# Performance work log

Hardware: AMD Instinct MI355X
Metric: run time of the kernel (lower is better)

The kernel has to match this reference:

```python
import jax, jax.numpy as jnp
import numpy as np

B, S, D = 2, 2048, 1024
H = 16
DH = D // H


def _layernorm(x, g, b, eps=1e-5):
    mu = jnp.mean(x, axis=-1, keepdims=True)
    var = jnp.var(x, axis=-1, keepdims=True)
    return (x - mu) * jax.lax.rsqrt(var + eps) * g + b


def setup_inputs() -> dict:
    key = jax.random.key(0)
    ks = jax.random.split(key, 8)
    s = lambda fan_in: 1.0 / np.sqrt(fan_in)
    return {
        "x": jax.random.normal(ks[0], (B, S, D), dtype=jnp.float32),
        "ln1_g": jnp.ones((D,), jnp.float32),
        "ln1_b": jnp.zeros((D,), jnp.float32),
        "w_qkv": jax.random.uniform(ks[1], (D, 3 * D), jnp.float32, -s(D), s(D)),
        "b_qkv": jnp.zeros((3 * D,), jnp.float32),
        "w_out": jax.random.uniform(ks[2], (D, D), jnp.float32, -s(D), s(D)),
        "b_out": jnp.zeros((D,), jnp.float32),
        "ln2_g": jnp.ones((D,), jnp.float32),
        "ln2_b": jnp.zeros((D,), jnp.float32),
        "w1": jax.random.uniform(ks[3], (D, 4 * D), jnp.float32, -s(D), s(D)),
        "b1": jnp.zeros((4 * D,), jnp.float32),
        "w2": jax.random.uniform(ks[4], (4 * D, D), jnp.float32, -s(4 * D), s(4 * D)),
        "b2": jnp.zeros((D,), jnp.float32),
    }


def reference(x, ln1_g, ln1_b, w_qkv, b_qkv, w_out, b_out,
              ln2_g, ln2_b, w1, b1, w2, b2):
    scale = DH ** -0.5
    residual = x
    h = _layernorm(x, ln1_g, ln1_b)
    qkv = h @ w_qkv + b_qkv                      # [B,S,3D]
    q, k, v = jnp.split(qkv, 3, axis=-1)
    # [B,S,D] -> [B,H,S,DH]
    split_heads = lambda t: t.reshape(B, S, H, DH).transpose(0, 2, 1, 3)
    q, k, v = map(split_heads, (q, k, v))
    scores = jnp.einsum("bhsd,bhtd->bhst", q, k) * scale  # full O(S^2) matrix
    attn = jax.nn.softmax(scores, axis=-1)
    out = jnp.einsum("bhst,bhtd->bhsd", attn, v)
    out = out.transpose(0, 2, 1, 3).reshape(B, S, D)
    out = out @ w_out + b_out                    # dropout is identity at eval
    x = residual + out
    residual = x
    h = _layernorm(x, ln2_g, ln2_b)
    h = jax.nn.gelu(h @ w1 + b1, approximate=False)
    h = h @ w2 + b2
    return residual + h
```

## Files before the change

kernel.cpp:

```cpp
#include <hip/hip_runtime.h>
#include <hip/hip_bf16.h>
#include <math.h>

#define Bc 2
#define Sc 2048
#define Dc 1024
#define Hc 16
#define DHc 64
#define Mc (Bc*Sc)

typedef __attribute__((ext_vector_type(8))) short bf16x8;
typedef __attribute__((ext_vector_type(4))) float f32x4;

#define QSCALE 0.18033688f

__device__ __forceinline__ ushort f2bf(float f){
  union { float f; uint32_t u; } c; c.f = f;
  uint32_t u = c.u;
  return (ushort)((u + 0x7fffu + ((u >> 16) & 1u)) >> 16);
}
__device__ __forceinline__ float fast_exp2(float x){
#if __has_builtin(__builtin_amdgcn_exp2f)
  return __builtin_amdgcn_exp2f(x);
#else
  return exp2f(x);
#endif
}
__device__ __forceinline__ float fast_rcp(float x){
#if __has_builtin(__builtin_amdgcn_rcpf)
  return __builtin_amdgcn_rcpf(x);
#else
  return 1.0f / x;
#endif
}
__device__ __forceinline__ float fast_gelu(float x){
  float x2 = x * x;
  float y  = x * (2.30220826f + 0.10294442f * x2);
  float t  = fast_exp2(fminf(y, 80.f));
  return x * t * fast_rcp(t + 1.0f);
}
__device__ __forceinline__ uint32_t cvt_pk_bf16(float a, float b){
  uint32_t r;
  asm("v_cvt_pk_bf16_f32 %0, %1, %2" : "=v"(r) : "v"(a), "v"(b));
  return r;
}

__device__ __forceinline__ void stage16(const void* g, void* lbase, int lane){
#if __has_builtin(__builtin_amdgcn_global_load_lds)
  __builtin_amdgcn_global_load_lds(
      (const __attribute__((address_space(1))) void*)g,
      (__attribute__((address_space(3))) void*)lbase, 16, 0, 0);
#else
  *(int4*)((char*)lbase + lane*16) = *(const int4*)g;
#endif
}

__global__ __launch_bounds__(256) void tcast(const float* __restrict__ w,
                                             ushort* __restrict__ wt,
                                             int K, int N){
  __shared__ float t[32][33];
  int kb = blockIdx.y * 32, nb = blockIdx.x * 32;
  int tx = threadIdx.x & 31, ty = threadIdx.x >> 5;
  #pragma unroll
  for (int i = 0; i < 4; i++)
    t[ty + 8*i][tx] = w[(size_t)(kb + ty + 8*i) * N + nb + tx];
  __syncthreads();
  #pragma unroll
  for (int i = 0; i < 4; i++)
    wt[(size_t)(nb + ty + 8*i) * K + kb + tx] = f2bf(t[tx][ty + 8*i]);
}

__global__ __launch_bounds__(256) void ln_bf16(const float* __restrict__ x,
                                               const float* __restrict__ g,
                                               const float* __restrict__ b,
                                               ushort* __restrict__ out){
  int row = blockIdx.x;
  const float4 xv = reinterpret_cast<const float4*>(x + (size_t)row * Dc)[threadIdx.x];
  float s  = xv.x + xv.y + xv.z + xv.w;
  float sq = xv.x*xv.x + xv.y*xv.y + xv.z*xv.z + xv.w*xv.w;
  #pragma unroll
  for (int m = 1; m < 64; m <<= 1){ s += __shfl_xor(s, m); sq += __shfl_xor(sq, m); }
  __shared__ float ss[4], ssq[4];
  int wv = threadIdx.x >> 6;
  if ((threadIdx.x & 63) == 0){ ss[wv] = s; ssq[wv] = sq; }
  __syncthreads();
  s  = ss[0] + ss[1] + ss[2] + ss[3];
  sq = ssq[0] + ssq[1] + ssq[2] + ssq[3];
  float mu  = s * (1.0f / Dc);
  float var = sq * (1.0f / Dc) - mu * mu;
  float rstd = rsqrtf(var + 1e-5f);
  float4 gv = reinterpret_cast<const float4*>(g)[threadIdx.x];
  float4 bv = reinterpret_cast<const float4*>(b)[threadIdx.x];
  ushort o[4];
  o[0] = f2bf((xv.x - mu) * rstd * gv.x + bv.x);
  o[1] = f2bf((xv.y - mu) * rstd * gv.y + bv.y);
  o[2] = f2bf((xv.z - mu) * rstd * gv.z + bv.z);
  o[3] = f2bf((xv.w - mu) * rstd * gv.w + bv.w);
  *reinterpret_cast<uint2*>(out + (size_t)row * Dc + threadIdx.x * 4) =
      *reinterpret_cast<uint2*>(o);
}

template<int EPI>
__global__ __launch_bounds__(256) void gemm128(
    const ushort* __restrict__ A, const ushort* __restrict__ BT,
    const float* __restrict__ bias,
    ushort* __restrict__ outb,
    ushort* __restrict__ oq, ushort* __restrict__ ok, ushort* __restrict__ ov,
    int N, int K){
  __shared__ short As[2][128*64];
  __shared__ short Bs[2][128*64];

  const int fid = blockIdx.x;
  const int q8 = gridDim.x >> 3;
  const int id2 = (fid & 7) * q8 + (fid >> 3);
  const int nbx = N / 128;
  const int nb = id2 % nbx, mb = id2 / nbx;

  const int tid = threadIdx.x;
  const int wave = tid >> 6, lane = tid & 63;
  const int wm = wave >> 1, wn = wave & 1;
  const int lr = lane & 15, lg = lane >> 4;

  f32x4 acc[4][4] = {};

  const int srow = wave * 8 + (lane >> 3);
  const int sgc  = ((lane & 7) ^ (lane >> 3)) * 8;
  const ushort* Ag = A  + (size_t)(mb * 128 + srow) * K + sgc;
  const ushort* Bg = BT + (size_t)(nb * 128 + srow) * K + sgc;
  const int nK = K >> 6;

  {
    char* Ab = (char*)&As[0][0] + wave * 1024;
    char* Bb = (char*)&Bs[0][0] + wave * 1024;
    #pragma unroll
    for (int c = 0; c < 4; c++){
      stage16(Ag + (size_t)c * 32 * K, Ab + c * 4096, lane);
      stage16(Bg + (size_t)c * 32 * K, Bb + c * 4096, lane);
    }
  }
  __syncthreads();

  const int swzr = (lr & 7) * 8;

  for (int kt = 0; kt < nK; ++kt){
    const int cur = kt & 1;
    if (kt + 1 < nK){
      const int ko = (kt + 1) * 64;
      char* Ab = (char*)&As[cur ^ 1][0] + wave * 1024;
      char* Bb = (char*)&Bs[cur ^ 1][0] + wave * 1024;
      #pragma unroll
      for (int c = 0; c < 4; c++){
        stage16(Ag + (size_t)c * 32 * K + ko, Ab + c * 4096, lane);
        stage16(Bg + (size_t)c * 32 * K + ko, Bb + c * 4096, lane);
      }
    }
    #pragma unroll
    for (int ks = 0; ks < 2; ks++){
      const int col = (ks * 32 + lg * 8) ^ swzr;
      bf16x8 af[4], bfr[4];
      #pragma unroll
      for (int mt = 0; mt < 4; mt++)
        af[mt] = *reinterpret_cast<const bf16x8*>(&As[cur][(wm*64 + mt*16 + lr)*64 + col]);
      #pragma unroll
      for (int nt = 0; nt < 4; nt++)
        bfr[nt] = *reinterpret_cast<const bf16x8*>(&Bs[cur][(wn*64 + nt*16 + lr)*64 + col]);
      #pragma unroll
      for (int mt = 0; mt < 4; mt++)
        #pragma unroll
        for (int nt = 0; nt < 4; nt++)
          acc[mt][nt] = __builtin_amdgcn_mfma_f32_16x16x32_bf16(af[mt], bfr[nt], acc[mt][nt], 0, 0, 0);
    }
    __syncthreads();
  }

  if (EPI == 0){
    #pragma unroll
    for (int mt = 0; mt < 4; mt++){
      const int gm0 = mb * 128 + wm * 64 + mt * 16 + lg * 4;
      const int bb = gm0 >> 11, s0 = gm0 & 2047;
      #pragma unroll
      for (int nt = 0; nt < 4; nt++){
        const int gn = nb * 128 + wn * 64 + nt * 16 + lr;
        const float bv = bias[gn];
        const int p = gn >> 10, d = gn & 1023;
        const int hh = d >> 6, dh = d & 63;
        const int bh = bb * Hc + hh;
        if (p == 2){
          ushort pk[4];
          #pragma unroll
          for (int r = 0; r < 4; r++) pk[r] = f2bf(acc[mt][nt][r] + bv);
          *reinterpret_cast<uint2*>(ov + ((size_t)bh * DHc + dh) * Sc + s0) =
              *reinterpret_cast<uint2*>(pk);
        } else if (p == 0){
          #pragma unroll
          for (int r = 0; r < 4; r++)
            oq[((size_t)bh * Sc + s0 + r) * DHc + dh] = f2bf((acc[mt][nt][r] + bv) * QSCALE);
        } else {
          #pragma unroll
          for (int r = 0; r < 4; r++)
            ok[((size_t)bh * Sc + s0 + r) * DHc + dh] = f2bf(acc[mt][nt][r] + bv);
        }
      }
    }
  } else {
    #pragma unroll
    for (int mt = 0; mt < 4; mt++){
      #pragma unroll
      for (int nt = 0; nt < 4; nt++){
        #pragma unroll
        for (int r = 0; r < 4; r++){
          const int gm = mb * 128 + wm * 64 + mt * 16 + lg * 4 + r;
          const int gn = nb * 128 + wn * 64 + nt * 16 + lr;
          outb[(size_t)gm * N + gn] = f2bf(fast_gelu(acc[mt][nt][r] + bias[gn]));
        }
      }
    }
  }
}

__global__ __launch_bounds__(256) void gemm_res64(
    const ushort* __restrict__ A, const ushort* __restrict__ BT,
    const float* __restrict__ bias, const float* __restrict__ res,
    float* __restrict__ outf, int N, int K){
  __shared__ short As[2][128*64];
  __shared__ short Bs[2][64*64];

  const int fid = blockIdx.x;
  const int q8 = gridDim.x >> 3;
  const int id2 = (fid & 7) * q8 + (fid >> 3);
  const int nbx = N / 64;
  const int nb = id2 % nbx, mb = id2 / nbx;

  const int tid = threadIdx.x;
  const int wave = tid >> 6, lane = tid & 63;
  const int wm = wave >> 1, wn = wave & 1;
  const int lr = lane & 15, lg = lane >> 4;

  f32x4 acc[4][2] = {};

  const int srow = wave * 8 + (lane >> 3);
  const int sgc  = ((lane & 7) ^ (lane >> 3)) * 8;
  const ushort* Ag = A  + (size_t)(mb * 128 + srow) * K + sgc;
  const ushort* Bg = BT + (size_t)(nb * 64  + srow) * K + sgc;
  const int nK = K >> 6;

  {
    char* Ab = (char*)&As[0][0] + wave * 1024;
    char* Bb = (char*)&Bs[0][0] + wave * 1024;
    #pragma unroll
    for (int c = 0; c < 4; c++)
      stage16(Ag + (size_t)c * 32 * K, Ab + c * 4096, lane);
    #pragma unroll
    for (int c = 0; c < 2; c++)
      stage16(Bg + (size_t)c * 32 * K, Bb + c * 4096, lane);
  }
  __syncthreads();

  const int swzr = (lr & 7) * 8;

  for (int kt = 0; kt < nK; ++kt){
    const int cur = kt & 1;
    if (kt + 1 < nK){
      const int ko = (kt + 1) * 64;
      char* Ab = (char*)&As[cur ^ 1][0] + wave * 1024;
      char* Bb = (char*)&Bs[cur ^ 1][0] + wave * 1024;
      #pragma unroll
      for (int c = 0; c < 4; c++)
        stage16(Ag + (size_t)c * 32 * K + ko, Ab + c * 4096, lane);
      #pragma unroll
      for (int c = 0; c < 2; c++)
        stage16(Bg + (size_t)c * 32 * K + ko, Bb + c * 4096, lane);
    }
    #pragma unroll
    for (int ks = 0; ks < 2; ks++){
      const int col = (ks * 32 + lg * 8) ^ swzr;
      bf16x8 af[4], bfr[2];
      #pragma unroll
      for (int mt = 0; mt < 4; mt++)
        af[mt] = *reinterpret_cast<const bf16x8*>(&As[cur][(wm*64 + mt*16 + lr)*64 + col]);
      #pragma unroll
      for (int nt = 0; nt < 2; nt++)
        bfr[nt] = *reinterpret_cast<const bf16x8*>(&Bs[cur][(wn*32 + nt*16 + lr)*64 + col]);
      #pragma unroll
      for (int mt = 0; mt < 4; mt++)
        #pragma unroll
        for (int nt = 0; nt < 2; nt++)
          acc[mt][nt] = __builtin_amdgcn_mfma_f32_16x16x32_bf16(af[mt], bfr[nt], acc[mt][nt], 0, 0, 0);
    }
    __syncthreads();
  }

  #pragma unroll
  for (int mt = 0; mt < 4; mt++){
    #pragma unroll
    for (int nt = 0; nt < 2; nt++){
      #pragma unroll
      for (int r = 0; r < 4; r++){
        const int gm = mb * 128 + wm * 64 + mt * 16 + lg * 4 + r;
        const int gn = nb * 64 + wn * 32 + nt * 16 + lr;
        const size_t i = (size_t)gm * N + gn;
        outf[i] = acc[mt][nt][r] + bias[gn] + res[i];
      }
    }
  }
}

__global__ __launch_bounds__(256) void flash_attn(const ushort* __restrict__ q,
                                                  const ushort* __restrict__ k,
                                                  const ushort* __restrict__ vt,
                                                  ushort* __restrict__ ctx){
  const int bh = blockIdx.y;
  const int q0 = blockIdx.x * 64;
  const int b  = bh >> 4, h = bh & 15;
  const int tid = threadIdx.x, wave = tid >> 6, lane = tid & 63;
  const int lr = lane & 15, lg = lane >> 4;

  __shared__ short Kt[2][64*64];
  __shared__ short Vt[64*64];
  __shared__ short Ps[4][16][68];

  const int g8  = lane & 7;
  const int kr0 = wave * 8 + (lane >> 3);
  const int kcol = (g8 ^ (kr0 & 7)) * 8;
  const ushort* kg0 = k + (size_t)bh * Sc * DHc + (size_t)kr0 * DHc + kcol;
  const ushort* kg1 = kg0 + 32 * DHc;
  char* Kl = (char*)&Kt[0][0] + wave * 1024;
  const int KBUFB = 64 * 64 * 2;

  const int vrow = tid >> 3, vg8 = tid & 7;
  const int vcol = (vg8 ^ (vrow & 7)) * 8;
  const ushort* vg0 = vt + (size_t)bh * DHc * Sc + (size_t)vrow * Sc + vcol;
  const ushort* vg1 = vg0 + (size_t)32 * Sc;

  bf16x8 qf0, qf1;
  {
    const ushort* qp = q + (size_t)bh * Sc * DHc + (size_t)(q0 + wave * 16 + lr) * DHc + lg * 8;
    qf0 = *reinterpret_cast<const bf16x8*>(qp);
    qf1 = *reinterpret_cast<const bf16x8*>(qp + 32);
  }

  f32x4 o[4] = {};
  float lps = 0.f;
  constexpr int NTILES = Sc / 64;

  stage16(kg0, Kl,        lane);
  stage16(kg1, Kl + 4096, lane);
  {
    int4 w0 = *reinterpret_cast<const int4*>(vg0);
    int4 w1 = *reinterpret_cast<const int4*>(vg1);
    *reinterpret_cast<int4*>((char*)&Vt[0] + tid * 16)        = w0;
    *reinterpret_cast<int4*>((char*)&Vt[0] + 4096 + tid * 16) = w1;
  }
  __syncthreads();

  const int swz = (lr & 7) * 8;

  for (int kt = 0; kt < NTILES; ++kt){
    const int cur = kt & 1;
    int4 vr0, vr1;
    if (kt + 1 < NTILES){
      const int nx = (cur ^ 1) * KBUFB;
      stage16(kg0 + (size_t)(kt + 1) * 64 * DHc, Kl + nx,        lane);
      stage16(kg1 + (size_t)(kt + 1) * 64 * DHc, Kl + nx + 4096, lane);
      vr0 = *reinterpret_cast<const int4*>(vg0 + (kt + 1) * 64);
      vr1 = *reinterpret_cast<const int4*>(vg1 + (kt + 1) * 64);
    }

    f32x4 sacc[4];
    __builtin_amdgcn_s_setprio(1);
    #pragma unroll
    for (int nt = 0; nt < 4; nt++){
      const int rb = (nt * 16 + lr) * 64;
      bf16x8 b0 = *reinterpret_cast<const bf16x8*>(&Kt[cur][rb + ((lg * 8) ^ swz)]);
      bf16x8 b1 = *reinterpret_cast<const bf16x8*>(&Kt[cur][rb + ((32 + lg * 8) ^ swz)]);
      f32x4 z = {0.f, 0.f, 0.f, 0.f};
      z = __builtin_amdgcn_mfma_f32_16x16x32_bf16(b0, qf0, z, 0, 0, 0);
      z = __builtin_amdgcn_mfma_f32_16x16x32_bf16(b1, qf1, z, 0, 0, 0);
      sacc[nt] = z;
    }
    __builtin_amdgcn_s_setprio(0);

    #pragma unroll
    for (int nt = 0; nt < 4; nt++){
      float p0 = fast_exp2(sacc[nt][0]);
      float p1 = fast_exp2(sacc[nt][1]);
      float p2 = fast_exp2(sacc[nt][2]);
      float p3 = fast_exp2(sacc[nt][3]);
      lps += (p0 + p1) + (p2 + p3);
      uint2 wd;
      wd.x = cvt_pk_bf16(p0, p1);
      wd.y = cvt_pk_bf16(p2, p3);
      *reinterpret_cast<uint2*>(&Ps[wave][lr][nt * 16 + lg * 4]) = wd;
    }

    bf16x8 pf0 = *reinterpret_cast<const bf16x8*>(&Ps[wave][lr][lg * 8]);
    bf16x8 pf1 = *reinterpret_cast<const bf16x8*>(&Ps[wave][lr][32 + lg * 8]);
    __builtin_amdgcn_s_setprio(1);
    #pragma unroll
    for (int nt = 0; nt < 4; nt++){
      const int rb = (nt * 16 + lr) * 64;
      bf16x8 v0 = *reinterpret_cast<const bf16x8*>(&Vt[rb + ((lg * 8) ^ swz)]);
      bf16x8 v1 = *reinterpret_cast<const bf16x8*>(&Vt[rb + ((32 + lg * 8) ^ swz)]);
      o[nt] = __builtin_amdgcn_mfma_f32_16x16x32_bf16(pf0, v0, o[nt], 0, 0, 0);
      o[nt] = __builtin_amdgcn_mfma_f32_16x16x32_bf16(pf1, v1, o[nt], 0, 0, 0);
    }
    __builtin_amdgcn_s_setprio(0);

    __syncthreads();
    if (kt + 1 < NTILES){
      *reinterpret_cast<int4*>((char*)&Vt[0] + tid * 16)        = vr0;
      *reinterpret_cast<int4*>((char*)&Vt[0] + 4096 + tid * 16) = vr1;
      __syncthreads();
    }
  }

  lps += __shfl_xor(lps, 16);
  lps += __shfl_xor(lps, 32);

  #pragma unroll
  for (int j = 0; j < 4; j++){
    float inv = 1.0f / __shfl(lps, lg * 4 + j);
    int s = q0 + wave * 16 + lg * 4 + j;
    ushort* op = ctx + ((size_t)b * Sc + s) * Dc + h * DHc;
    #pragma unroll
    for (int nt = 0; nt < 4; nt++)
      op[nt * 16 + lr] = f2bf(o[nt][j] * inv);
  }
}

extern "C" void kernel_launch(void* const* d_in, const int* in_sizes, int n_in,
                              void* d_out, int out_size, void* d_ws, size_t ws_size,
                              hipStream_t stream){
  const float* x     = (const float*)d_in[0];
  const float* ln1_g = (const float*)d_in[1];
  const float* ln1_b = (const float*)d_in[2];
  const float* w_qkv = (const float*)d_in[3];
  const float* b_qkv = (const float*)d_in[4];
  const float* w_out = (const float*)d_in[5];
  const float* b_out = (const float*)d_in[6];
  const float* ln2_g = (const float*)d_in[7];
  const float* ln2_b = (const float*)d_in[8];
  const float* w1    = (const float*)d_in[9];
  const float* b1    = (const float*)d_in[10];
  const float* w2    = (const float*)d_in[11];
  const float* b2    = (const float*)d_in[12];
  float* out = (float*)d_out;

  char* ws = (char*)d_ws;
  size_t off = 0;
  ushort* wqkvT = (ushort*)(ws + off); off += (size_t)3072 * 1024 * 2;
  ushort* woutT = (ushort*)(ws + off); off += (size_t)1024 * 1024 * 2;
  ushort* w1T   = (ushort*)(ws + off); off += (size_t)4096 * 1024 * 2;
  ushort* w2T   = (ushort*)(ws + off); off += (size_t)1024 * 4096 * 2;
  ushort* hln   = (ushort*)(ws + off); off += (size_t)Mc * Dc * 2;
  ushort* qbuf  = (ushort*)(ws + off); off += (size_t)32 * Sc * DHc * 2;
  ushort* kbuf  = (ushort*)(ws + off); off += (size_t)32 * Sc * DHc * 2;
  ushort* vtbuf = (ushort*)(ws + off); off += (size_t)32 * Sc * DHc * 2;
  ushort* ctx   = (ushort*)(ws + off); off += (size_t)Mc * Dc * 2;
  float*  x1    = (float*)(ws + off);  off += (size_t)Mc * Dc * 4;
  ushort* act   = qbuf;

  tcast<<<dim3(3072 / 32, 1024 / 32), 256, 0, stream>>>(w_qkv, wqkvT, 1024, 3072);
  tcast<<<dim3(1024 / 32, 1024 / 32), 256, 0, stream>>>(w_out, woutT, 1024, 1024);
  tcast<<<dim3(4096 / 32, 1024 / 32), 256, 0, stream>>>(w1,    w1T,   1024, 4096);
  tcast<<<dim3(1024 / 32, 4096 / 32), 256, 0, stream>>>(w2,    w2T,   4096, 1024);

  ln_bf16<<<Mc, 256, 0, stream>>>(x, ln1_g, ln1_b, hln);

  gemm128<0><<<(3072/128) * (Mc/128), 256, 0, stream>>>(
      hln, wqkvT, b_qkv, nullptr, qbuf, kbuf, vtbuf, 3072, 1024);

  flash_attn<<<dim3(Sc / 64, 32), 256, 0, stream>>>(qbuf, kbuf, vtbuf, ctx);

  gemm_res64<<<(1024/64) * (Mc/128), 256, 0, stream>>>(
      ctx, woutT, b_out, x, x1, 1024, 1024);

  ln_bf16<<<Mc, 256, 0, stream>>>(x1, ln2_g, ln2_b, hln);

  gemm128<2><<<(4096/128) * (Mc/128), 256, 0, stream>>>(
      hln, w1T, b1, act, nullptr, nullptr, nullptr, 4096, 1024);

  gemm_res64<<<(1024/64) * (Mc/128), 256, 0, stream>>>(
      act, w2T, b2, x1, out, 1024, 4096);
}
```

Before: 250.4 us.

## Triple-buffer residual GEMM loads and double per-block query rows in attention

The residual GEMM moves from a double-buffered to a triple-buffered LDS pipeline, prefetching two tiles ahead. It waits on outstanding loads with explicit vmcnt counts and a single barrier per iteration, which removes the trailing syncthreads. The flash attention kernel now gives each wave 32 query rows instead of 16, so each staged K/V tile serves twice as many queries and the grid is halved. This trades extra LDS and registers, and therefore possibly lower occupancy and fewer blocks (512), for less K/V reload traffic and fewer barriers.

After: 251.6 us. Within noise of the previous version (+0.5%).

```diff
diff --git a/kernel.cpp b/kernel.cpp
--- a/kernel.cpp
+++ b/kernel.cpp
@@ -222,8 +222,8 @@
     const ushort* __restrict__ A, const ushort* __restrict__ BT,
     const float* __restrict__ bias, const float* __restrict__ res,
     float* __restrict__ outf, int N, int K){
-  __shared__ short As[2][128*64];
-  __shared__ short Bs[2][64*64];
+  __shared__ short As[3][128*64];
+  __shared__ short Bs[3][64*64];
 
   const int fid = blockIdx.x;
   const int q8 = gridDim.x >> 3;
@@ -244,32 +244,31 @@
   const ushort* Bg = BT + (size_t)(nb * 64  + srow) * K + sgc;
   const int nK = K >> 6;
 
-  {
-    char* Ab = (char*)&As[0][0] + wave * 1024;
-    char* Bb = (char*)&Bs[0][0] + wave * 1024;
+  auto stage_tile = [&](int t, int bi){
+    const int ko = t * 64;
+    char* Ab = (char*)&As[bi][0] + wave * 1024;
+    char* Bb = (char*)&Bs[bi][0] + wave * 1024;
     #pragma unroll
     for (int c = 0; c < 4; c++)
-      stage16(Ag + (size_t)c * 32 * K, Ab + c * 4096, lane);
+      stage16(Ag + (size_t)c * 32 * K + ko, Ab + c * 4096, lane);
     #pragma unroll
     for (int c = 0; c < 2; c++)
-      stage16(Bg + (size_t)c * 32 * K, Bb + c * 4096, lane);
-  }
-  __syncthreads();
+      stage16(Bg + (size_t)c * 32 * K + ko, Bb + c * 4096, lane);
+  };
+
+  stage_tile(0, 0);
+  stage_tile(1, 1);
 
   const int swzr = (lr & 7) * 8;
+  int cur = 0;
 
   for (int kt = 0; kt < nK; ++kt){
-    const int cur = kt & 1;
-    if (kt + 1 < nK){
-      const int ko = (kt + 1) * 64;
-      char* Ab = (char*)&As[cur ^ 1][0] + wave * 1024;
-      char* Bb = (char*)&Bs[cur ^ 1][0] + wave * 1024;
-      #pragma unroll
-      for (int c = 0; c < 4; c++)
-        stage16(Ag + (size_t)c * 32 * K + ko, Ab + c * 4096, lane);
-      #pragma unroll
-      for (int c = 0; c < 2; c++)
-        stage16(Bg + (size_t)c * 32 * K + ko, Bb + c * 4096, lane);
+    if (kt + 1 < nK) asm volatile("s_waitcnt vmcnt(6)" ::: "memory");
+    else             asm volatile("s_waitcnt vmcnt(0)" ::: "memory");
+    __builtin_amdgcn_s_barrier();
+    if (kt + 2 < nK){
+      int nxt = cur + 2; if (nxt >= 3) nxt -= 3;
+      stage_tile(kt + 2, nxt);
     }
     #pragma unroll
     for (int ks = 0; ks < 2; ks++){
@@ -287,7 +286,7 @@
         for (int nt = 0; nt < 2; nt++)
           acc[mt][nt] = __builtin_amdgcn_mfma_f32_16x16x32_bf16(af[mt], bfr[nt], acc[mt][nt], 0, 0, 0);
     }
-    __syncthreads();
+    cur += 1; if (cur >= 3) cur -= 3;
   }
 
   #pragma unroll
@@ -310,14 +309,14 @@
                                                   const ushort* __restrict__ vt,
                                                   ushort* __restrict__ ctx){
   const int bh = blockIdx.y;
-  const int q0 = blockIdx.x * 64;
+  const int q0 = blockIdx.x * 128;
   const int b  = bh >> 4, h = bh & 15;
   const int tid = threadIdx.x, wave = tid >> 6, lane = tid & 63;
   const int lr = lane & 15, lg = lane >> 4;
 
   __shared__ short Kt[2][64*64];
   __shared__ short Vt[64*64];
-  __shared__ short Ps[4][16][68];
+  __shared__ short Ps[4][32][68];
 
   const int g8  = lane & 7;
   const int kr0 = wave * 8 + (lane >> 3);
@@ -332,15 +331,17 @@
   const ushort* vg0 = vt + (size_t)bh * DHc * Sc + (size_t)vrow * Sc + vcol;
   const ushort* vg1 = vg0 + (size_t)32 * Sc;
 
-  bf16x8 qf0, qf1;
-  {
-    const ushort* qp = q + (size_t)bh * Sc * DHc + (size_t)(q0 + wave * 16 + lr) * DHc + lg * 8;
-    qf0 = *reinterpret_cast<const bf16x8*>(qp);
-    qf1 = *reinterpret_cast<const bf16x8*>(qp + 32);
-  }
-
-  f32x4 o[4] = {};
-  float lps = 0.f;
+  bf16x8 qf[2][2];
+  #pragma unroll
+  for (int qi = 0; qi < 2; qi++){
+    const ushort* qp = q + (size_t)bh * Sc * DHc
+                         + (size_t)(q0 + wave * 32 + qi * 16 + lr) * DHc + lg * 8;
+    qf[qi][0] = *reinterpret_cast<const bf16x8*>(qp);
+    qf[qi][1] = *reinterpret_cast<const bf16x8*>(qp + 32);
+  }
+
+  f32x4 o[2][4] = {};
+  float lps[2] = {0.f, 0.f};
   constexpr int NTILES = Sc / 64;
 
   stage16(kg0, Kl,        lane);
@@ -366,43 +367,56 @@
       vr1 = *reinterpret_cast<const int4*>(vg1 + (kt + 1) * 64);
     }
 
-    f32x4 sacc[4];
+    f32x4 sacc[2][4];
     __builtin_amdgcn_s_setprio(1);
     #pragma unroll
     for (int nt = 0; nt < 4; nt++){
       const int rb = (nt * 16 + lr) * 64;
       bf16x8 b0 = *reinterpret_cast<const bf16x8*>(&Kt[cur][rb + ((lg * 8) ^ swz)]);
       bf16x8 b1 = *reinterpret_cast<const bf16x8*>(&Kt[cur][rb + ((32 + lg * 8) ^ swz)]);
-      f32x4 z = {0.f, 0.f, 0.f, 0.f};
-      z = __builtin_amdgcn_mfma_f32_16x16x32_bf16(b0, qf0, z, 0, 0, 0);
-      z = __builtin_amdgcn_mfma_f32_16x16x32_bf16(b1, qf1, z, 0, 0, 0);
-      sacc[nt] = z;
+      #pragma unroll
+      for (int qi = 0; qi < 2; qi++){
+        f32x4 z = {0.f, 0.f, 0.f, 0.f};
+        z = __builtin_amdgcn_mfma_f32_16x16x32_bf16(b0, qf[qi][0], z, 0, 0, 0);
+        z = __builtin_amdgcn_mfma_f32_16x16x32_bf16(b1, qf[qi][1], z, 0, 0, 0);
+        sacc[qi][nt] = z;
+      }
     }
     __builtin_amdgcn_s_setprio(0);
 
     #pragma unroll
-    for (int nt = 0; nt < 4; nt++){
-      float p0 = fast_exp2(sacc[nt][0]);
-      float p1 = fast_exp2(sacc[nt][1]);
-      float p2 = fast_exp2(sacc[nt][2]);
-      float p3 = fast_exp2(sacc[nt][3]);
-      lps += (p0 + p1) + (p2 + p3);
-      uint2 wd;
-      wd.x = cvt_pk_bf16(p0, p1);
-      wd.y = cvt_pk_bf16(p2, p3);
-      *reinterpret_cast<uint2*>(&Ps[wave][lr][nt * 16 + lg * 4]) = wd;
-    }
-
-    bf16x8 pf0 = *reinterpret_cast<const bf16x8*>(&Ps[wave][lr][lg * 8]);
-    bf16x8 pf1 = *reinterpret_cast<const bf16x8*>(&Ps[wave][lr][32 + lg * 8]);
+    for (int qi = 0; qi < 2; qi++){
+      #pragma unroll
+      for (int nt = 0; nt < 4; nt++){
+        float p0 = fast_exp2(sacc[qi][nt][0]);
+        float p1 = fast_exp2(sacc[qi][nt][1]);
+        float p2 = fast_exp2(sacc[qi][nt][2]);
+        float p3 = fast_exp2(sacc[qi][nt][3]);
+        lps[qi] += (p0 + p1) + (p2 + p3);
+        uint2 wd;
+        wd.x = cvt_pk_bf16(p0, p1);
+        wd.y = cvt_pk_bf16(p2, p3);
+        *reinterpret_cast<uint2*>(&Ps[wave][qi * 16 + lr][nt * 16 + lg * 4]) = wd;
+      }
+    }
+
+    bf16x8 pf[2][2];
+    #pragma unroll
+    for (int qi = 0; qi < 2; qi++){
+      pf[qi][0] = *reinterpret_cast<const bf16x8*>(&Ps[wave][qi * 16 + lr][lg * 8]);
+      pf[qi][1] = *reinterpret_cast<const bf16x8*>(&Ps[wave][qi * 16 + lr][32 + lg * 8]);
+    }
     __builtin_amdgcn_s_setprio(1);
     #pragma unroll
     for (int nt = 0; nt < 4; nt++){
       const int rb = (nt * 16 + lr) * 64;
       bf16x8 v0 = *reinterpret_cast<const bf16x8*>(&Vt[rb + ((lg * 8) ^ swz)]);
       bf16x8 v1 = *reinterpret_cast<const bf16x8*>(&Vt[rb + ((32 + lg * 8) ^ swz)]);
-      o[nt] = __builtin_amdgcn_mfma_f32_16x16x32_bf16(pf0, v0, o[nt], 0, 0, 0);
-      o[nt] = __builtin_amdgcn_mfma_f32_16x16x32_bf16(pf1, v1, o[nt], 0, 0, 0);
+      #pragma unroll
+      for (int qi = 0; qi < 2; qi++){
+        o[qi][nt] = __builtin_amdgcn_mfma_f32_16x16x32_bf16(pf[qi][0], v0, o[qi][nt], 0, 0, 0);
+        o[qi][nt] = __builtin_amdgcn_mfma_f32_16x16x32_bf16(pf[qi][1], v1, o[qi][nt], 0, 0, 0);
+      }
     }
     __builtin_amdgcn_s_setprio(0);
 
@@ -414,17 +428,20 @@
     }
   }
 
-  lps += __shfl_xor(lps, 16);
-  lps += __shfl_xor(lps, 32);
-
   #pragma unroll
-  for (int j = 0; j < 4; j++){
-    float inv = 1.0f / __shfl(lps, lg * 4 + j);
-    int s = q0 + wave * 16 + lg * 4 + j;
-    ushort* op = ctx + ((size_t)b * Sc + s) * Dc + h * DHc;
-    #pragma unroll
-    for (int nt = 0; nt < 4; nt++)
-      op[nt * 16 + lr] = f2bf(o[nt][j] * inv);
+  for (int qi = 0; qi < 2; qi++){
+    float l = lps[qi];
+    l += __shfl_xor(l, 16);
+    l += __shfl_xor(l, 32);
+    #pragma unroll
+    for (int j = 0; j < 4; j++){
+      float inv = 1.0f / __shfl(l, lg * 4 + j);
+      int s = q0 + wave * 32 + qi * 16 + lg * 4 + j;
+      ushort* op = ctx + ((size_t)b * Sc + s) * Dc + h * DHc;
+      #pragma unroll
+      for (int nt = 0; nt < 4; nt++)
+        op[nt * 16 + lr] = f2bf(o[qi][nt][j] * inv);
+    }
   }
 }
 
@@ -470,7 +487,7 @@
   gemm128<0><<<(3072/128) * (Mc/128), 256, 0, stream>>>(
       hln, wqkvT, b_qkv, nullptr, qbuf, kbuf, vtbuf, 3072, 1024);
 
-  flash_attn<<<dim3(Sc / 64, 32), 256, 0, stream>>>(qbuf, kbuf, vtbuf, ctx);
+  flash_attn<<<dim3(Sc / 128, 32), 256, 0, stream>>>(qbuf, kbuf, vtbuf, ctx);
 
   gemm_res64<<<(1024/64) * (Mc/128), 256, 0, stream>>>(
       ctx, woutT, b_out, x, x1, 1024, 1024);
```
